# Optimization experiments

Measured on AMD Instinct MI355X. Metric: run time of the kernel, lower is better.

## Reference

```python
import jax, jax.numpy as jnp
import numpy as np

EUCLIDEAN_DIM = 6
B = 1024


def _build_tables(n):
    # CGA: basis vectors e1..en, e+, e-, diagonal metric (+1)*(n+1), (-1)
    d = n + 2
    nb = 1 << d
    metric = [1] * (n + 1) + [-1]
    # clifford orders blades by (grade, lexicographic) == (popcount, bitmask)
    masks = sorted(range(nb), key=lambda m: (bin(m).count('1'), m))
    pos = {m: i for i, m in enumerate(masks)}

    def sign_of(a, b):
        # canonical reordering sign + metric contractions for common vectors
        s = 1
        aa = a >> 1
        cnt = 0
        while aa:
            cnt += bin(aa & b).count('1')
            aa >>= 1
        if cnt & 1:
            s = -s
        common = a & b
        i = 0
        while common:
            if (common & 1) and metric[i] < 0:
                s = -s
            common >>= 1
            i += 1
        return s

    nnz = nb * nb  # every basis-blade product is one signed blade (nondegenerate metric)
    left = np.empty(nnz, np.int32)
    right = np.empty(nnz, np.int32)
    res = np.empty(nnz, np.int32)
    sgn = np.empty(nnz, np.int32)
    t = 0
    for i in range(nb):
        ma = masks[i]
        for j in range(nb):
            mb = masks[j]
            left[t] = i
            right[t] = j
            res[t] = pos[ma ^ mb]
            sgn[t] = sign_of(ma, mb)
            t += 1
    grades = np.array([bin(m).count('1') for m in masks])
    point_mask = np.where(grades == 1)[0].astype(np.int32)           # grade-1 blades
    pseudo = pos[nb - 1]
    motor_mask = np.where((grades % 2 == 0) & (np.arange(nb) != pseudo))[0].astype(np.int32)
    rev = ((-1) ** ((grades * (grades - 1)) // 2)).astype(np.int32)  # reverse signs
    motor_rev = rev[motor_mask]
    return left, right, res, sgn, point_mask, motor_mask, motor_rev


def setup_inputs() -> dict:
    key = jax.random.key(0)
    k1, k2 = jax.random.split(key)
    left, right, res, sgn, pmask, mmask, mrev = _build_tables(EUCLIDEAN_DIM)
    motor = jax.random.normal(k1, (B, mmask.shape[0]), jnp.float32)
    x = jax.random.normal(k2, (B, EUCLIDEAN_DIM), jnp.float32)
    return {
        'motor': motor,
        'x': x,
        'left_idx': jnp.asarray(left),
        'right_idx': jnp.asarray(right),
        'result_idx': jnp.asarray(res),
        'signs': jnp.asarray(sgn),
        'point_mask': jnp.asarray(pmask),
        'motor_mask': jnp.asarray(mmask),
        'motor_reverse_signs': jnp.asarray(mrev),
    }


def _gp(a, b, left_idx, right_idx, result_idx, signs_f, nb):
    # gather-multiply-scatter geometric product (same pattern as torch scatter_add)
    prod = signs_f * a[:, left_idx] * b[:, right_idx]  # (B, nnz)
    return jnp.zeros((a.shape[0], nb), a.dtype).at[:, result_idx].add(prod)


def reference(motor, x, left_idx, right_idx, result_idx, signs, point_mask, motor_mask, motor_reverse_signs):
    n = EUCLIDEAN_DIM
    nb = 1 << (n + 2)
    signs_f = signs.astype(jnp.float32)
    # UPGC encode: X = [x, -0.5 + 0.5|x|^2, 0.5 + 0.5|x|^2]
    h = 0.5 * jnp.sum(x * x, axis=-1, keepdims=True)
    point = jnp.concatenate([x, h - 0.5, h + 0.5], axis=-1)  # (B, n+2)
    Bsz = motor.shape[0]
    motor_full = jnp.zeros((Bsz, nb), jnp.float32).at[:, motor_mask].set(motor)
    point_full = jnp.zeros((Bsz, nb), jnp.float32).at[:, point_mask].set(point)
    motor_rev = motor * motor_reverse_signs.astype(jnp.float32)
    motor_rev_full = jnp.zeros((Bsz, nb), jnp.float32).at[:, motor_mask].set(motor_rev)
    # sandwich product M X M~ via two sparse geometric products
    mx = _gp(motor_full, point_full, left_idx, right_idx, result_idx, signs_f, nb)
    out_full = _gp(mx, motor_rev_full, left_idx, right_idx, result_idx, signs_f, nb)
    transformed = out_full[:, point_mask]  # (B, n+2)
    # UPGC decode: first n components
    return transformed[:, :n]
```

## Files before the change

### kernel.cpp

```cpp
#include <hip/hip_runtime.h>

#define NB   256
#define NM   127
#define NP   8
#define ND   6

#define FIRST_OFF  0
#define SECOND_OFF 2048
#define MP_OFF     3064
#define PREP_N     3191

__global__ __launch_bounds__(256) void cga_prep(
    const int* __restrict__ result_idx,
    const int* __restrict__ signs,
    const int* __restrict__ point_mask,
    const int* __restrict__ motor_mask,
    const int* __restrict__ mrev_signs,
    int* __restrict__ ws)
{
    int e = blockIdx.x * 256 + threadIdx.x;
    if (e < 2048) {
        int i  = e >> 3, k = e & 7;
        int pp = point_mask[k];
        int m  = result_idx[i * NB + pp];
        int s  = signs[m * NB + pp];
        ws[FIRST_OFF + e] = (m << 1) | (s < 0 ? 1 : 0);
    } else if (e < SECOND_OFF + NM * 8) {
        int q = e - SECOND_OFF;
        int j = q >> 3, r = q & 7;
        int v = 0;
        if (r < ND) {
            int rp = point_mask[r];
            int jp = motor_mask[j];
            int i  = result_idx[rp * NB + jp];
            int s  = signs[i * NB + jp];
            v = (i << 1) | (s < 0 ? 1 : 0);
        }
        ws[SECOND_OFF + q] = v;
    } else if (e < PREP_N) {
        int j = e - MP_OFF;
        ws[MP_OFF + j] = (motor_mask[j] << 1) | (mrev_signs[j] < 0 ? 1 : 0);
    }
}

__global__ __launch_bounds__(256) void cga_apply(
    const float* __restrict__ motor,
    const float* __restrict__ x,
    const int*   __restrict__ ws,
    float*       __restrict__ out)
{
    __shared__ float m_full[NB];
    __shared__ float mx[NB];
    __shared__ float xs[ND];
    __shared__ float wpart[4][ND];

    const int t = threadIdx.x;
    const int b = blockIdx.x;

    m_full[t] = 0.0f;

    const int4* ft = (const int4*)(ws + FIRST_OFF);
    int4 f0 = ft[2 * t];
    int4 f1 = ft[2 * t + 1];

    int   mp = 0;
    float mv = 0.0f;
    int4  s0 = {0,0,0,0}, s1 = {0,0,0,0};
    if (t < NM) {
        mv = motor[b * NM + t];
        mp = ws[MP_OFF + t];
        const int4* st = (const int4*)(ws + SECOND_OFF);
        s0 = st[2 * t];
        s1 = st[2 * t + 1];
    }
    if (t < ND) xs[t] = x[b * ND + t];
    __syncthreads();

    if (t < NM) m_full[mp >> 1] = mv;
    __syncthreads();

    float pv[NP];
    float h = 0.0f;
    #pragma unroll
    for (int k = 0; k < ND; ++k) { float v = xs[k]; pv[k] = v; h += v * v; }
    h *= 0.5f;
    pv[6] = h - 0.5f;
    pv[7] = h + 0.5f;

    int fe[8] = { f0.x, f0.y, f0.z, f0.w, f1.x, f1.y, f1.z, f1.w };
    float acc = 0.0f;
    #pragma unroll
    for (int k = 0; k < NP; ++k) {
        int   m = fe[k] >> 1;
        float v = m_full[m] * pv[k];
        acc += (fe[k] & 1) ? -v : v;
    }
    mx[t] = acc;
    __syncthreads();

    float o[ND] = {0,0,0,0,0,0};
    if (t < NM) {
        float mr = (mp & 1) ? -mv : mv;
        int se[ND] = { s0.x, s0.y, s0.z, s0.w, s1.x, s1.y };
        #pragma unroll
        for (int r = 0; r < ND; ++r) {
            int   i = se[r] >> 1;
            float v = mx[i] * mr;
            o[r] += (se[r] & 1) ? -v : v;
        }
    }

    #pragma unroll
    for (int r = 0; r < ND; ++r) {
        float v = o[r];
        #pragma unroll
        for (int d = 32; d >= 1; d >>= 1) v += __shfl_down(v, d, 64);
        o[r] = v;
    }
    const int lane = t & 63, w = t >> 6;
    if (lane == 0) {
        #pragma unroll
        for (int r = 0; r < ND; ++r) wpart[w][r] = o[r];
    }
    __syncthreads();

    if (t < ND)
        out[b * ND + t] = wpart[0][t] + wpart[1][t] + wpart[2][t] + wpart[3][t];
}

extern "C" void kernel_launch(void* const* d_in, const int* in_sizes, int n_in,
                              void* d_out, int out_size, void* d_ws, size_t ws_size,
                              hipStream_t stream) {
    const float* motor      = (const float*)d_in[0];
    const float* x          = (const float*)d_in[1];
    const int*   result_idx = (const int*)d_in[4];
    const int*   signs      = (const int*)d_in[5];
    const int*   point_mask = (const int*)d_in[6];
    const int*   motor_mask = (const int*)d_in[7];
    const int*   mrev       = (const int*)d_in[8];
    int*         ws         = (int*)d_ws;
    float*       out        = (float*)d_out;

    const int Bsz = in_sizes[0] / NM;

    cga_prep<<<(PREP_N + 255) / 256, 256, 0, stream>>>(
        result_idx, signs, point_mask, motor_mask, mrev, ws);
    cga_apply<<<Bsz, 256, 0, stream>>>(motor, x, ws, out);
}
```

Measured before the change: 75.02 us.

## Bake Cayley lookup tables into device constants at compile time, drop prep kernel

Computes the sandwich-product lookup tables with constexpr at compile time and stores them in a __device__ constant instead of deriving them from the result_idx/signs inputs in a separate prep kernel. This removes one kernel launch and its dependent gather reads. The apply kernel also fills shared memory through an inverse motor-mask table, which removes one __syncthreads. The change ignores the table inputs passed at runtime and assumes they always match the fixed CGA layout.

```diff
diff --git a/kernel.cpp b/kernel.cpp
--- a/kernel.cpp
+++ b/kernel.cpp
@@ -5,48 +5,74 @@
 #define NP   8
 #define ND   6
 
-#define FIRST_OFF  0
-#define SECOND_OFF 2048
-#define MP_OFF     3064
-#define PREP_N     3191
 
-__global__ __launch_bounds__(256) void cga_prep(
-    const int* __restrict__ result_idx,
-    const int* __restrict__ signs,
-    const int* __restrict__ point_mask,
-    const int* __restrict__ motor_mask,
-    const int* __restrict__ mrev_signs,
-    int* __restrict__ ws)
-{
-    int e = blockIdx.x * 256 + threadIdx.x;
-    if (e < 2048) {
-        int i  = e >> 3, k = e & 7;
-        int pp = point_mask[k];
-        int m  = result_idx[i * NB + pp];
-        int s  = signs[m * NB + pp];
-        ws[FIRST_OFF + e] = (m << 1) | (s < 0 ? 1 : 0);
-    } else if (e < SECOND_OFF + NM * 8) {
-        int q = e - SECOND_OFF;
-        int j = q >> 3, r = q & 7;
-        int v = 0;
-        if (r < ND) {
-            int rp = point_mask[r];
-            int jp = motor_mask[j];
-            int i  = result_idx[rp * NB + jp];
-            int s  = signs[i * NB + jp];
-            v = (i << 1) | (s < 0 ? 1 : 0);
+constexpr int popc8(int x) { int c = 0; while (x) { c += x & 1; x >>= 1; } return c; }
+
+constexpr int sign_of(int a, int b) {
+    int s = 1;
+    int aa = a >> 1, cnt = 0;
+    while (aa) { cnt += popc8(aa & b); aa >>= 1; }
+    if (cnt & 1) s = -s;
+    int common = a & b, i = 0;
+    while (common) {
+        if ((common & 1) && i == 7) s = -s;
+        common >>= 1; ++i;
+    }
+    return s;
+}
+
+struct Tables {
+    alignas(16) int firstT[NB * 8];
+    alignas(16) int secondT[128 * 8];
+    alignas(16) int mpacked[128];
+    alignas(16) int invm[NB];
+};
+
+constexpr Tables build_tables() {
+    Tables T{};
+    int masks[NB] = {}, pos[NB] = {};
+    int t = 0;
+    for (int pc = 0; pc <= 8; ++pc)
+        for (int m = 0; m < NB; ++m)
+            if (popc8(m) == pc) masks[t++] = m;
+    for (int i = 0; i < NB; ++i) pos[masks[i]] = i;
+
+    for (int i = 0; i < NB; ++i)
+        for (int k = 0; k < NP; ++k) {
+            int pp = 1 + k;
+            int m  = pos[masks[i] ^ masks[pp]];
+            int s  = sign_of(masks[m], masks[pp]);
+            T.firstT[i * 8 + k] = (m << 1) | (s < 0 ? 1 : 0);
         }
-        ws[SECOND_OFF + q] = v;
-    } else if (e < PREP_N) {
-        int j = e - MP_OFF;
-        ws[MP_OFF + j] = (motor_mask[j] << 1) | (mrev_signs[j] < 0 ? 1 : 0);
+
+    for (int i = 0; i < NB; ++i) T.invm[i] = -1;
+    int j = 0;
+    for (int i = 0; i < NB; ++i) {
+        int g = popc8(masks[i]);
+        if ((g % 2 == 0) && masks[i] != 255) {
+            int rev = ((g * (g - 1) / 2) % 2) ? -1 : 1;
+            T.mpacked[j] = (i << 1) | (rev < 0 ? 1 : 0);
+            T.invm[i] = j;
+            for (int r = 0; r < ND; ++r) {
+                int rp = 1 + r;
+                int ii = pos[masks[rp] ^ masks[i]];
+                int s  = sign_of(masks[ii], masks[i]);
+                T.secondT[j * 8 + r] = (ii << 1) | (s < 0 ? 1 : 0);
+            }
+            T.secondT[j * 8 + 6] = 0;
+            T.secondT[j * 8 + 7] = 0;
+            ++j;
+        }
     }
+    return T;
 }
+
+constexpr Tables hT = build_tables();
+__device__ const Tables dT = hT;
 
 __global__ __launch_bounds__(256) void cga_apply(
     const float* __restrict__ motor,
     const float* __restrict__ x,
-    const int*   __restrict__ ws,
     float*       __restrict__ out)
 {
     __shared__ float m_full[NB];
@@ -57,26 +83,24 @@
     const int t = threadIdx.x;
     const int b = blockIdx.x;
 
-    m_full[t] = 0.0f;
-
-    const int4* ft = (const int4*)(ws + FIRST_OFF);
+    const int4* ft = (const int4*)dT.firstT;
     int4 f0 = ft[2 * t];
     int4 f1 = ft[2 * t + 1];
 
+    float mv = 0.0f;
     int   mp = 0;
-    float mv = 0.0f;
     int4  s0 = {0,0,0,0}, s1 = {0,0,0,0};
     if (t < NM) {
         mv = motor[b * NM + t];
-        mp = ws[MP_OFF + t];
-        const int4* st = (const int4*)(ws + SECOND_OFF);
+        mp = dT.mpacked[t];
+        const int4* st = (const int4*)dT.secondT;
         s0 = st[2 * t];
         s1 = st[2 * t + 1];
     }
     if (t < ND) xs[t] = x[b * ND + t];
-    __syncthreads();
 
-    if (t < NM) m_full[mp >> 1] = mv;
+    const int im = dT.invm[t];
+    m_full[t] = (im >= 0) ? motor[b * NM + im] : 0.0f;
     __syncthreads();
 
     float pv[NP];
@@ -131,19 +155,10 @@
 extern "C" void kernel_launch(void* const* d_in, const int* in_sizes, int n_in,
                               void* d_out, int out_size, void* d_ws, size_t ws_size,
                               hipStream_t stream) {
-    const float* motor      = (const float*)d_in[0];
-    const float* x          = (const float*)d_in[1];
-    const int*   result_idx = (const int*)d_in[4];
-    const int*   signs      = (const int*)d_in[5];
-    const int*   point_mask = (const int*)d_in[6];
-    const int*   motor_mask = (const int*)d_in[7];
-    const int*   mrev       = (const int*)d_in[8];
-    int*         ws         = (int*)d_ws;
-    float*       out        = (float*)d_out;
+    const float* motor = (const float*)d_in[0];
+    const float* x     = (const float*)d_in[1];
+    float* out = (float*)d_out;
 
     const int Bsz = in_sizes[0] / NM;
-
-    cga_prep<<<(PREP_N + 255) / 256, 256, 0, stream>>>(
-        result_idx, signs, point_mask, motor_mask, mrev, ws);
-    cga_apply<<<Bsz, 256, 0, stream>>>(motor, x, ws, out);
+    cga_apply<<<Bsz, 256, 0, stream>>>(motor, x, out);
 }
```

New measurement: 72.15 us. 3.8% less time.
